# Kernel optimization log

Measured on AMD Instinct MI355X. Metric: run time of the kernel, lower is better.

The kernel has to match this reference:

```python
import jax, jax.numpy as jnp
import numpy as np

HEAD_DIM = 64
FEAT_H, FEAT_W = 64, 64
ROPE_THETA = 10000.0


def axial_rope_cache(dim, height, width, theta):
    # Matches compute_axial_rope_cache: interleaved cos/sin of shape [H*W, dim]
    theta_dim = (dim // 2) // 2
    freqs = 1.0 / theta ** (jnp.arange(theta_dim, dtype=jnp.float32) * 2.0 / theta_dim)
    t_x = jnp.tile(jnp.arange(width, dtype=jnp.float32)[None, :], (height, 1)).reshape(-1)
    t_y = jnp.tile(jnp.arange(height, dtype=jnp.float32)[:, None], (1, width)).reshape(-1)
    theta_all = jnp.concatenate([jnp.outer(t_x, freqs), jnp.outer(t_y, freqs)], axis=-1)
    cos = jnp.repeat(jnp.cos(theta_all), 2, axis=-1)  # [H*W, dim]
    sin = jnp.repeat(jnp.sin(theta_all), 2, axis=-1)
    return cos, sin


def apply_rope(x, cos, sin):
    # x: [B, H, N, D]; cos/sin: [N, D]
    x1 = x[..., 0::2]
    x2 = x[..., 1::2]
    rot = jnp.stack([-x2, x1], axis=-1).reshape(x.shape)
    return x * cos[None, None] + rot * sin[None, None]


def setup_inputs() -> dict:
    key = jax.random.key(0)
    ks = jax.random.split(key, 11)
    B, Nq, Nk, E, KVD, ID = 1, 4096, 8192, 256, 64, 256
    s_e = 1.0 / np.sqrt(E)
    s_kv = 1.0 / np.sqrt(KVD)
    s_i = 1.0 / np.sqrt(ID)
    return {
        "query": jax.random.normal(ks[0], (B, Nq, E), jnp.float32),
        "key": jax.random.normal(ks[1], (B, Nk, KVD), jnp.float32),
        "value": jax.random.normal(ks[2], (B, Nk, KVD), jnp.float32),
        "Wq": jax.random.normal(ks[3], (E, ID), jnp.float32) * s_e,
        "bq": jnp.zeros((ID,), jnp.float32),
        "Wk": jax.random.normal(ks[4], (KVD, ID), jnp.float32) * s_kv,
        "bk": jnp.zeros((ID,), jnp.float32),
        "Wv": jax.random.normal(ks[5], (KVD, ID), jnp.float32) * s_kv,
        "bv": jnp.zeros((ID,), jnp.float32),
        "Wo": jax.random.normal(ks[6], (ID, E), jnp.float32) * s_i,
        "bo": jnp.zeros((E,), jnp.float32),
        "num_k_exclude_rope": 0,
    }


def reference(query, key, value, Wq, bq, Wk, bk, Wv, bv, Wo, bo, num_k_exclude_rope):
    B, Nq, _ = query.shape
    Nk = key.shape[1]
    H, D = 4, HEAD_DIM

    def split_heads(x):
        b, n, c = x.shape
        return x.reshape(b, n, H, c // H).transpose(0, 2, 1, 3)

    q = split_heads(query @ Wq + bq)  # [B,H,Nq,D]
    k = split_heads(key @ Wk + bk)    # [B,H,Nk,D]
    v = split_heads(value @ Wv + bv)

    cos, sin = axial_rope_cache(D, FEAT_H, FEAT_W, ROPE_THETA)  # [4096, D]
    q = apply_rope(q, cos, sin)

    num_k_rope = Nk - num_k_exclude_rope
    k_spatial = k[:, :, :num_k_rope, :]
    k_other = k[:, :, num_k_rope:, :]
    repeats = num_k_rope // cos.shape[0]  # rope_k_repeat=True
    cos_k = jnp.tile(cos, (repeats, 1))
    sin_k = jnp.tile(sin, (repeats, 1))
    k_spatial = apply_rope(k_spatial, cos_k, sin_k)
    k = jnp.concatenate([k_spatial, k_other], axis=2)

    q = q / jnp.sqrt(jnp.asarray(D, q.dtype))
    scores = jnp.einsum("bhqd,bhkd->bhqk", q, k)
    attn = jax.nn.softmax(scores, axis=-1)
    out = jnp.einsum("bhqk,bhkd->bhqd", attn, v)
    out = out.transpose(0, 2, 1, 3).reshape(B, Nq, H * D)
    return out @ Wo + bo
```

## Files before the change

kernel.cpp:

```cpp
#include <hip/hip_runtime.h>
#include <hip/hip_bf16.h>

#define H 4
#define NQ 4096
#define NK 8192
#define D 64
#define BK 64
#define NSPLIT 8
#define KSPAN (NK / NSPLIT)
#define PST 72

#define QSCALE 0.1803368801111204f

typedef short v8s __attribute__((ext_vector_type(8)));
typedef float v4f __attribute__((ext_vector_type(4)));

static __device__ __forceinline__ unsigned short f2bf(float f) {
    unsigned int u = __float_as_uint(f);
    u = (u + 0x7FFFu + ((u >> 16) & 1u)) >> 16;
    return (unsigned short)u;
}
static __device__ __forceinline__ float bf2f(unsigned short h) {
    return __uint_as_float(((unsigned int)h) << 16);
}
static __device__ __forceinline__ unsigned int pkbf(float a, float b) {
    union { __hip_bfloat162 h; unsigned int u; } cv;
    cv.h = __float22bfloat162_rn(make_float2(a, b));
    return cv.u;
}
static __device__ __forceinline__ void split8(const float* a, v8s& hi, v8s& lo) {
#pragma unroll
    for (int j = 0; j < 8; ++j) {
        unsigned short h = f2bf(a[j]);
        hi[j] = (short)h;
        lo[j] = (short)f2bf(a[j] - bf2f(h));
    }
}
static __device__ __forceinline__ void dma16(const unsigned short* g, unsigned short* l) {
    __builtin_amdgcn_global_load_lds(
        (const __attribute__((address_space(1))) unsigned int*)(const void*)g,
        (__attribute__((address_space(3))) unsigned int*)(void*)l, 16, 0, 0);
}

__global__ __launch_bounds__(256) void wprep_kernel(
    const float* __restrict__ Wq, const float* __restrict__ Wk,
    const float* __restrict__ Wv, const float* __restrict__ Wo,
    unsigned short* __restrict__ Wqt, unsigned short* __restrict__ Wkt,
    unsigned short* __restrict__ Wvt, unsigned short* __restrict__ Wot)
{
    int i = blockIdx.x * 256 + threadIdx.x;
    const float* src; unsigned short* dst; int idx, sh;
    if (i < 65536)       { src = Wq; dst = Wqt; idx = i;          sh = 8; }
    else if (i < 81920)  { src = Wk; dst = Wkt; idx = i - 65536;  sh = 6; }
    else if (i < 98304)  { src = Wv; dst = Wvt; idx = i - 81920;  sh = 6; }
    else                 { src = Wo; dst = Wot; idx = i - 98304;  sh = 8; }
    const int K = 1 << sh;
    const int c = idx >> sh, e = idx & (K - 1);
    const float v = src[e * 256 + c];
    const unsigned short h = f2bf(v);
    dst[idx] = h;
    dst[idx + (K << 8)] = f2bf(v - bf2f(h));
}

__global__ __launch_bounds__(256) void qkv_kernel(
    const float* __restrict__ query, const float* __restrict__ key,
    const float* __restrict__ value,
    const unsigned short* __restrict__ Wqt, const unsigned short* __restrict__ Wkt,
    const unsigned short* __restrict__ Wvt,
    const float* __restrict__ bq, const float* __restrict__ bk,
    const float* __restrict__ bv,
    unsigned short* __restrict__ Qb, unsigned short* __restrict__ Kb,
    unsigned short* __restrict__ Vt, const int* __restrict__ nexp)
{
    const int b = blockIdx.x;
    const int t = threadIdx.x, w = t >> 6, lane = t & 63;
    const int quad = lane >> 4, l16 = lane & 15;
    const int colbase = w * 64;

    if (b < 128) {
        const int n0 = b * 32;
        v4f acc[2][4];
#pragma unroll
        for (int st = 0; st < 2; ++st)
#pragma unroll
            for (int ct = 0; ct < 4; ++ct) {
                const float bb = bq[colbase + ct * 16 + l16];
                acc[st][ct] = v4f{bb, bb, bb, bb};
            }
#pragma unroll
        for (int k0 = 0; k0 < 256; k0 += 32) {
            v8s ah[2], al[2];
#pragma unroll
            for (int st = 0; st < 2; ++st) {
                float av[8];
                const float* ar = query + (size_t)(n0 + st * 16 + l16) * 256 + k0 + quad * 8;
                *(float4*)av = *(const float4*)ar;
                *(float4*)(av + 4) = *(const float4*)(ar + 4);
                split8(av, ah[st], al[st]);
            }
#pragma unroll
            for (int ct = 0; ct < 4; ++ct) {
                const unsigned short* wp = Wqt + (size_t)(colbase + ct * 16 + l16) * 256 + k0 + quad * 8;
                const v8s wh = *(const v8s*)wp;
                const v8s wl = *(const v8s*)(wp + 65536);
#pragma unroll
                for (int st = 0; st < 2; ++st) {
                    acc[st][ct] = __builtin_amdgcn_mfma_f32_16x16x32_bf16(al[st], wh, acc[st][ct], 0, 0, 0);
                    acc[st][ct] = __builtin_amdgcn_mfma_f32_16x16x32_bf16(ah[st], wl, acc[st][ct], 0, 0, 0);
                    acc[st][ct] = __builtin_amdgcn_mfma_f32_16x16x32_bf16(ah[st], wh, acc[st][ct], 0, 0, 0);
                }
            }
        }
#pragma unroll
        for (int ct = 0; ct < 4; ++ct) {
            const int d = ct * 16 + l16;
            const int j = d >> 1;
            const float freq = exp2f(-(float)(j & 15) * 1.66096404744368f);
            const bool isx = (j < 16), odd = (d & 1);
#pragma unroll
            for (int st = 0; st < 2; ++st)
#pragma unroll
                for (int r = 0; r < 4; ++r) {
                    const int p = n0 + st * 16 + quad * 4 + r;
                    const float tpos = isx ? (float)(p & 63) : (float)(p >> 6);
                    float sn, cs;
                    __sincosf(tpos * freq, &sn, &cs);
                    const float x = acc[st][ct][r];
                    const float xp = __shfl_xor(x, 1, 64);
                    const float y = odd ? fmaf(x, cs, xp * sn) : fmaf(x, cs, -xp * sn);
                    Qb[((size_t)(w * NQ + p) << 6) + d] = f2bf(y * QSCALE);
                }
        }
    } else {
        const bool isK = (b < 384);
        const int n0 = (isK ? (b - 128) : (b - 384)) * 32;
        const float* X = isK ? key : value;
        const unsigned short* Wt = isK ? Wkt : Wvt;
        const float* bias = isK ? bk : bv;
        v8s wf[4][2][2];
#pragma unroll
        for (int ct = 0; ct < 4; ++ct)
#pragma unroll
            for (int k = 0; k < 2; ++k) {
                const unsigned short* wp = Wt + (size_t)(colbase + ct * 16 + l16) * 64 + k * 32 + quad * 8;
                wf[ct][k][0] = *(const v8s*)wp;
                wf[ct][k][1] = *(const v8s*)(wp + 16384);
            }
        v4f acc[2][4];
#pragma unroll
        for (int st = 0; st < 2; ++st)
#pragma unroll
            for (int ct = 0; ct < 4; ++ct) {
                const float bb = bias[colbase + ct * 16 + l16];
                acc[st][ct] = v4f{bb, bb, bb, bb};
            }
#pragma unroll
        for (int st = 0; st < 2; ++st)
#pragma unroll
            for (int k = 0; k < 2; ++k) {
                float av[8];
                const float* ar = X + (size_t)(n0 + st * 16 + l16) * 64 + k * 32 + quad * 8;
                *(float4*)av = *(const float4*)ar;
                *(float4*)(av + 4) = *(const float4*)(ar + 4);
                v8s ah, al;
                split8(av, ah, al);
#pragma unroll
                for (int ct = 0; ct < 4; ++ct) {
                    acc[st][ct] = __builtin_amdgcn_mfma_f32_16x16x32_bf16(al, wf[ct][k][0], acc[st][ct], 0, 0, 0);
                    acc[st][ct] = __builtin_amdgcn_mfma_f32_16x16x32_bf16(ah, wf[ct][k][1], acc[st][ct], 0, 0, 0);
                    acc[st][ct] = __builtin_amdgcn_mfma_f32_16x16x32_bf16(ah, wf[ct][k][0], acc[st][ct], 0, 0, 0);
                }
            }
        if (isK) {
            const int nro = NK - *nexp;
#pragma unroll
            for (int ct = 0; ct < 4; ++ct) {
                const int d = ct * 16 + l16;
                const int j = d >> 1;
                const float freq = exp2f(-(float)(j & 15) * 1.66096404744368f);
                const bool isx = (j < 16), odd = (d & 1);
#pragma unroll
                for (int st = 0; st < 2; ++st)
#pragma unroll
                    for (int r = 0; r < 4; ++r) {
                        const int p = n0 + st * 16 + quad * 4 + r;
                        const int pc = p & 4095;
                        const float tpos = isx ? (float)(pc & 63) : (float)(pc >> 6);
                        float sn, cs;
                        __sincosf(tpos * freq, &sn, &cs);
                        const float x = acc[st][ct][r];
                        const float xp = __shfl_xor(x, 1, 64);
                        float y = odd ? fmaf(x, cs, xp * sn) : fmaf(x, cs, -xp * sn);
                        y = (p < nro) ? y : x;
                        Kb[((size_t)(w * NK + p) << 6) + d] = f2bf(y);
                    }
            }
        } else {
#pragma unroll
            for (int ct = 0; ct < 4; ++ct) {
                const int col = colbase + ct * 16 + l16;
#pragma unroll
                for (int st = 0; st < 2; ++st) {
                    uint2 u = make_uint2(pkbf(acc[st][ct][0], acc[st][ct][1]),
                                         pkbf(acc[st][ct][2], acc[st][ct][3]));
                    *(uint2*)(Vt + (size_t)col * NK + n0 + st * 16 + quad * 4) = u;
                }
            }
        }
    }
}

__global__ __launch_bounds__(256) void attn_kernel(
    const unsigned short* __restrict__ Qb, const unsigned short* __restrict__ Kb,
    const unsigned short* __restrict__ Vt, unsigned short* __restrict__ Opart,
    float* __restrict__ Lbuf)
{
    __shared__ alignas(16) unsigned short Kl[64 * 64];
    __shared__ alignas(16) unsigned short Vl[64 * 64];
    __shared__ alignas(16) unsigned short Pl[4 * 32 * PST];

    const int blk = blockIdx.x;
    const int s = blk & 7, h = (blk >> 3) & 3, qt = blk >> 5;
    const int t = threadIdx.x;
    const int w = t >> 6, lane = t & 63;
    const int quad = lane >> 4, l16 = lane & 15;

    const int q0 = qt * 128 + w * 32;
    v8s qf[2][2];
#pragma unroll
    for (int g = 0; g < 2; ++g) {
        const unsigned short* qr = Qb + ((size_t)(h * NQ + q0 + g * 16 + l16) << 6) + quad * 8;
        qf[g][0] = *(const v8s*)qr;
        qf[g][1] = *(const v8s*)(qr + 32);
    }

    v4f O[4][2];
#pragma unroll
    for (int dt = 0; dt < 4; ++dt)
#pragma unroll
        for (int g = 0; g < 2; ++g) O[dt][g] = v4f{0.f, 0.f, 0.f, 0.f};
    float psum[2] = {0.f, 0.f};

    const unsigned short* Kbase = Kb + (((size_t)h * NK + s * KSPAN) << 6);
    const unsigned short* Vbase = Vt + (size_t)(h * 64) * NK + s * KSPAN;

    const int srow = lane >> 3;
    const int schunk = (lane & 7) ^ srow;
    const int c0off = ((quad ^ (l16 & 7)) * 8);
    const int c1off = c0off ^ 32;
    unsigned short* Pw = &Pl[w * 32 * PST];

    for (int k0 = 0; k0 < KSPAN; k0 += BK) {
        __syncthreads();
#pragma unroll
        for (int half = 0; half < 2; ++half) {
            const int r0 = w * 16 + half * 8;
            dma16(Kbase + ((size_t)(k0 + r0 + srow) << 6) + schunk * 8, &Kl[r0 * 64]);
            dma16(Vbase + (size_t)(r0 + srow) * NK + k0 + schunk * 8, &Vl[r0 * 64]);
        }
        __syncthreads();

#pragma unroll
        for (int tt = 0; tt < 4; ++tt) {
            const unsigned short* kr = &Kl[(tt * 16 + l16) * 64];
            const v8s kf0 = *(const v8s*)(kr + c0off);
            const v8s kf1 = *(const v8s*)(kr + c1off);
#pragma unroll
            for (int g = 0; g < 2; ++g) {
                v4f a = v4f{0.f, 0.f, 0.f, 0.f};
                a = __builtin_amdgcn_mfma_f32_16x16x32_bf16(kf0, qf[g][0], a, 0, 0, 0);
                a = __builtin_amdgcn_mfma_f32_16x16x32_bf16(kf1, qf[g][1], a, 0, 0, 0);
                const float e0 = __builtin_amdgcn_exp2f(a[0]);
                const float e1 = __builtin_amdgcn_exp2f(a[1]);
                const float e2 = __builtin_amdgcn_exp2f(a[2]);
                const float e3 = __builtin_amdgcn_exp2f(a[3]);
                psum[g] += (e0 + e1) + (e2 + e3);
                *(uint2*)(&Pw[(g * 16 + l16) * PST + tt * 16 + quad * 4]) =
                    make_uint2(pkbf(e0, e1), pkbf(e2, e3));
            }
        }
        __asm__ volatile("s_waitcnt lgkmcnt(0)" ::: "memory");

        v8s pf[2][2];
#pragma unroll
        for (int g = 0; g < 2; ++g) {
            const unsigned short* pr = &Pw[(g * 16 + l16) * PST + quad * 8];
            pf[g][0] = *(const v8s*)pr;
            pf[g][1] = *(const v8s*)(pr + 32);
        }
#pragma unroll
        for (int dt = 0; dt < 4; ++dt) {
            const unsigned short* vr = &Vl[(dt * 16 + l16) * 64];
            const v8s vf0 = *(const v8s*)(vr + c0off);
            const v8s vf1 = *(const v8s*)(vr + c1off);
#pragma unroll
            for (int g = 0; g < 2; ++g) {
                v4f a = O[dt][g];
                a = __builtin_amdgcn_mfma_f32_16x16x32_bf16(vf0, pf[g][0], a, 0, 0, 0);
                a = __builtin_amdgcn_mfma_f32_16x16x32_bf16(vf1, pf[g][1], a, 0, 0, 0);
                O[dt][g] = a;
            }
        }
    }

#pragma unroll
    for (int g = 0; g < 2; ++g) {
        float p = psum[g];
        p += __shfl_xor(p, 16, 64);
        p += __shfl_xor(p, 32, 64);
        psum[g] = p;
    }
    unsigned short* Ob = Opart + (size_t)blk * 8192;
#pragma unroll
    for (int g = 0; g < 2; ++g) {
        const int row = w * 32 + g * 16 + l16;
#pragma unroll
        for (int dt = 0; dt < 4; ++dt) {
            uint2 u = make_uint2(pkbf(O[dt][g][0], O[dt][g][1]),
                                 pkbf(O[dt][g][2], O[dt][g][3]));
            *(uint2*)(Ob + row * 64 + dt * 16 + quad * 4) = u;
        }
        if (quad == 0) Lbuf[blk * 128 + row] = psum[g];
    }
}

__global__ __launch_bounds__(256) void oproj_kernel(
    const unsigned short* __restrict__ Opart, const float* __restrict__ Lbuf,
    const unsigned short* __restrict__ Wt, const float* __restrict__ bo,
    float* __restrict__ out)
{
    const int t = threadIdx.x, w = t >> 6, lane = t & 63;
    const int quad = lane >> 4, l16 = lane & 15;
    const int n0 = blockIdx.x * 16, colbase = w * 64;
    const int qt = n0 >> 7, rbase = n0 & 127;

    v4f facc[4];
#pragma unroll
    for (int ct = 0; ct < 4; ++ct) facc[ct] = v4f{0.f, 0.f, 0.f, 0.f};

#pragma unroll 1
    for (int hh = 0; hh < 4; ++hh) {
        v8s wfr[4][2][2];
#pragma unroll
        for (int ct = 0; ct < 4; ++ct)
#pragma unroll
            for (int ch = 0; ch < 2; ++ch) {
                const unsigned short* wp = Wt + (size_t)(colbase + ct * 16 + l16) * 256 + hh * 64 + ch * 32 + quad * 8;
                wfr[ct][ch][0] = *(const v8s*)wp;
                wfr[ct][ch][1] = *(const v8s*)(wp + 65536);
            }
        v4f hacc[4];
#pragma unroll
        for (int ct = 0; ct < 4; ++ct) hacc[ct] = v4f{0.f, 0.f, 0.f, 0.f};
        float4 lsum = make_float4(0.f, 0.f, 0.f, 0.f);
#pragma unroll
        for (int sp = 0; sp < NSPLIT; ++sp) {
            const int slab = (qt * 4 + hh) * 8 + sp;
            const unsigned short* arow = Opart + (size_t)slab * 8192 + (rbase + l16) * 64;
#pragma unroll
            for (int ch = 0; ch < 2; ++ch) {
                const v8s A = *(const v8s*)(arow + ch * 32 + quad * 8);
#pragma unroll
                for (int ct = 0; ct < 4; ++ct) {
                    hacc[ct] = __builtin_amdgcn_mfma_f32_16x16x32_bf16(A, wfr[ct][ch][0], hacc[ct], 0, 0, 0);
                    hacc[ct] = __builtin_amdgcn_mfma_f32_16x16x32_bf16(A, wfr[ct][ch][1], hacc[ct], 0, 0, 0);
                }
            }
            const float4 lv = *(const float4*)(Lbuf + slab * 128 + rbase + quad * 4);
            lsum.x += lv.x; lsum.y += lv.y; lsum.z += lv.z; lsum.w += lv.w;
        }
        const float li[4] = {1.f / lsum.x, 1.f / lsum.y, 1.f / lsum.z, 1.f / lsum.w};
#pragma unroll
        for (int ct = 0; ct < 4; ++ct)
#pragma unroll
            for (int r = 0; r < 4; ++r)
                facc[ct][r] = fmaf(hacc[ct][r], li[r], facc[ct][r]);
    }
#pragma unroll
    for (int ct = 0; ct < 4; ++ct) {
        const float bb = bo[colbase + ct * 16 + l16];
#pragma unroll
        for (int r = 0; r < 4; ++r)
            out[(size_t)(n0 + quad * 4 + r) * 256 + colbase + ct * 16 + l16] = facc[ct][r] + bb;
    }
}

extern "C" void kernel_launch(void* const* d_in, const int* in_sizes, int n_in,
                              void* d_out, int out_size, void* d_ws, size_t ws_size,
                              hipStream_t stream) {
    const float* query = (const float*)d_in[0];
    const float* key   = (const float*)d_in[1];
    const float* value = (const float*)d_in[2];
    const float* Wq    = (const float*)d_in[3];
    const float* bq    = (const float*)d_in[4];
    const float* Wk    = (const float*)d_in[5];
    const float* bk    = (const float*)d_in[6];
    const float* Wv    = (const float*)d_in[7];
    const float* bv    = (const float*)d_in[8];
    const float* Wo    = (const float*)d_in[9];
    const float* bo    = (const float*)d_in[10];
    const int*   nex   = (const int*)d_in[11];

    char* ws = (char*)d_ws;
    unsigned short* Qb  = (unsigned short*)(ws);
    unsigned short* Kb  = (unsigned short*)(ws + (size_t)2  * 1024 * 1024);
    unsigned short* Vt  = (unsigned short*)(ws + (size_t)6  * 1024 * 1024);
    unsigned short* Opart = (unsigned short*)(ws + (size_t)10 * 1024 * 1024);
    float* Lbuf         = (float*)(ws + (size_t)26 * 1024 * 1024);
    char* wbase         = ws + (size_t)26 * 1024 * 1024 + 512 * 1024;
    unsigned short* Wqt = (unsigned short*)(wbase);
    unsigned short* Wkt = (unsigned short*)(wbase + 256 * 1024);
    unsigned short* Wvt = (unsigned short*)(wbase + 320 * 1024);
    unsigned short* Wot = (unsigned short*)(wbase + 384 * 1024);
    float* out          = (float*)d_out;

    wprep_kernel<<<640, 256, 0, stream>>>(Wq, Wk, Wv, Wo, Wqt, Wkt, Wvt, Wot);
    qkv_kernel<<<640, 256, 0, stream>>>(query, key, value, Wqt, Wkt, Wvt,
                                        bq, bk, bv, Qb, Kb, Vt, nex);
    attn_kernel<<<1024, 256, 0, stream>>>(Qb, Kb, Vt, Opart, Lbuf);
    oproj_kernel<<<256, 256, 0, stream>>>(Opart, Lbuf, Wot, bo, out);
}
```

Measured before the change: 180.2 us.

## Drop weight-prep kernel, gather fp32 weights inline, retile attention and output projection

Removes the separate weight transpose/split kernel. The QKV and output-projection kernels now gather the fp32 weights with strided loads and split them into bf16 hi/lo on the fly. The QKV grid halves rows per block (doubling the block count), and attention uses 128-thread blocks with 64 query rows per wave. The output projection uses 512 threads, splits the heads across two wave halves and reduces them through shared memory. This saves a kernel launch and its memory round-trip, but adds uncoalesced strided weight reads and redundant conversion work in every block.

```diff
diff --git a/kernel.cpp b/kernel.cpp
--- a/kernel.cpp
+++ b/kernel.cpp
@@ -1,13 +1,11 @@
 #include <hip/hip_runtime.h>
 #include <hip/hip_bf16.h>
 
-#define H 4
 #define NQ 4096
 #define NK 8192
-#define D 64
-#define BK 64
 #define NSPLIT 8
 #define KSPAN (NK / NSPLIT)
+#define BK 64
 #define PST 72
 
 #define QSCALE 0.1803368801111204f
@@ -36,37 +34,24 @@
         lo[j] = (short)f2bf(a[j] - bf2f(h));
     }
 }
+static __device__ __forceinline__ void wgather(const float* __restrict__ W,
+                                               int k0, int col, v8s& wh, v8s& wl) {
+    float wv[8];
+#pragma unroll
+    for (int j = 0; j < 8; ++j) wv[j] = W[(size_t)(k0 + j) * 256 + col];
+    split8(wv, wh, wl);
+}
 static __device__ __forceinline__ void dma16(const unsigned short* g, unsigned short* l) {
     __builtin_amdgcn_global_load_lds(
         (const __attribute__((address_space(1))) unsigned int*)(const void*)g,
         (__attribute__((address_space(3))) unsigned int*)(void*)l, 16, 0, 0);
 }
 
-__global__ __launch_bounds__(256) void wprep_kernel(
-    const float* __restrict__ Wq, const float* __restrict__ Wk,
-    const float* __restrict__ Wv, const float* __restrict__ Wo,
-    unsigned short* __restrict__ Wqt, unsigned short* __restrict__ Wkt,
-    unsigned short* __restrict__ Wvt, unsigned short* __restrict__ Wot)
-{
-    int i = blockIdx.x * 256 + threadIdx.x;
-    const float* src; unsigned short* dst; int idx, sh;
-    if (i < 65536)       { src = Wq; dst = Wqt; idx = i;          sh = 8; }
-    else if (i < 81920)  { src = Wk; dst = Wkt; idx = i - 65536;  sh = 6; }
-    else if (i < 98304)  { src = Wv; dst = Wvt; idx = i - 81920;  sh = 6; }
-    else                 { src = Wo; dst = Wot; idx = i - 98304;  sh = 8; }
-    const int K = 1 << sh;
-    const int c = idx >> sh, e = idx & (K - 1);
-    const float v = src[e * 256 + c];
-    const unsigned short h = f2bf(v);
-    dst[idx] = h;
-    dst[idx + (K << 8)] = f2bf(v - bf2f(h));
-}
-
 __global__ __launch_bounds__(256) void qkv_kernel(
     const float* __restrict__ query, const float* __restrict__ key,
     const float* __restrict__ value,
-    const unsigned short* __restrict__ Wqt, const unsigned short* __restrict__ Wkt,
-    const unsigned short* __restrict__ Wvt,
+    const float* __restrict__ Wq, const float* __restrict__ Wk,
+    const float* __restrict__ Wv,
     const float* __restrict__ bq, const float* __restrict__ bk,
     const float* __restrict__ bv,
     unsigned short* __restrict__ Qb, unsigned short* __restrict__ Kb,
@@ -77,38 +62,29 @@
     const int quad = lane >> 4, l16 = lane & 15;
     const int colbase = w * 64;
 
-    if (b < 128) {
-        const int n0 = b * 32;
-        v4f acc[2][4];
-#pragma unroll
-        for (int st = 0; st < 2; ++st)
+    if (b < 256) {
+        const int n0 = b * 16;
+        v4f acc[4];
+#pragma unroll
+        for (int ct = 0; ct < 4; ++ct) {
+            const float bb = bq[colbase + ct * 16 + l16];
+            acc[ct] = v4f{bb, bb, bb, bb};
+        }
+        const float* arow = query + (size_t)(n0 + l16) * 256 + quad * 8;
+#pragma unroll
+        for (int k0 = 0; k0 < 256; k0 += 32) {
+            float av[8];
+            *(float4*)av = *(const float4*)(arow + k0);
+            *(float4*)(av + 4) = *(const float4*)(arow + k0 + 4);
+            v8s ah, al;
+            split8(av, ah, al);
 #pragma unroll
             for (int ct = 0; ct < 4; ++ct) {
-                const float bb = bq[colbase + ct * 16 + l16];
-                acc[st][ct] = v4f{bb, bb, bb, bb};
-            }
-#pragma unroll
-        for (int k0 = 0; k0 < 256; k0 += 32) {
-            v8s ah[2], al[2];
-#pragma unroll
-            for (int st = 0; st < 2; ++st) {
-                float av[8];
-                const float* ar = query + (size_t)(n0 + st * 16 + l16) * 256 + k0 + quad * 8;
-                *(float4*)av = *(const float4*)ar;
-                *(float4*)(av + 4) = *(const float4*)(ar + 4);
-                split8(av, ah[st], al[st]);
-            }
-#pragma unroll
-            for (int ct = 0; ct < 4; ++ct) {
-                const unsigned short* wp = Wqt + (size_t)(colbase + ct * 16 + l16) * 256 + k0 + quad * 8;
-                const v8s wh = *(const v8s*)wp;
-                const v8s wl = *(const v8s*)(wp + 65536);
-#pragma unroll
-                for (int st = 0; st < 2; ++st) {
-                    acc[st][ct] = __builtin_amdgcn_mfma_f32_16x16x32_bf16(al[st], wh, acc[st][ct], 0, 0, 0);
-                    acc[st][ct] = __builtin_amdgcn_mfma_f32_16x16x32_bf16(ah[st], wl, acc[st][ct], 0, 0, 0);
-                    acc[st][ct] = __builtin_amdgcn_mfma_f32_16x16x32_bf16(ah[st], wh, acc[st][ct], 0, 0, 0);
-                }
+                v8s wh, wl;
+                wgather(Wq, k0 + quad * 8, colbase + ct * 16 + l16, wh, wl);
+                acc[ct] = __builtin_amdgcn_mfma_f32_16x16x32_bf16(al, wh, acc[ct], 0, 0, 0);
+                acc[ct] = __builtin_amdgcn_mfma_f32_16x16x32_bf16(ah, wl, acc[ct], 0, 0, 0);
+                acc[ct] = __builtin_amdgcn_mfma_f32_16x16x32_bf16(ah, wh, acc[ct], 0, 0, 0);
             }
         }
 #pragma unroll
@@ -118,59 +94,46 @@
             const float freq = exp2f(-(float)(j & 15) * 1.66096404744368f);
             const bool isx = (j < 16), odd = (d & 1);
 #pragma unroll
-            for (int st = 0; st < 2; ++st)
-#pragma unroll
-                for (int r = 0; r < 4; ++r) {
-                    const int p = n0 + st * 16 + quad * 4 + r;
-                    const float tpos = isx ? (float)(p & 63) : (float)(p >> 6);
-                    float sn, cs;
-                    __sincosf(tpos * freq, &sn, &cs);
-                    const float x = acc[st][ct][r];
-                    const float xp = __shfl_xor(x, 1, 64);
-                    const float y = odd ? fmaf(x, cs, xp * sn) : fmaf(x, cs, -xp * sn);
-                    Qb[((size_t)(w * NQ + p) << 6) + d] = f2bf(y * QSCALE);
-                }
+            for (int r = 0; r < 4; ++r) {
+                const int p = n0 + quad * 4 + r;
+                const float tpos = isx ? (float)(p & 63) : (float)(p >> 6);
+                float sn, cs;
+                __sincosf(tpos * freq, &sn, &cs);
+                const float x = acc[ct][r];
+                const float xp = __shfl_xor(x, 1, 64);
+                const float y = odd ? fmaf(x, cs, xp * sn) : fmaf(x, cs, -xp * sn);
+                Qb[((size_t)(w * NQ + p) << 6) + d] = f2bf(y * QSCALE);
+            }
         }
     } else {
-        const bool isK = (b < 384);
-        const int n0 = (isK ? (b - 128) : (b - 384)) * 32;
+        const bool isK = (b < 768);
+        const int n0 = (isK ? (b - 256) : (b - 768)) * 16;
         const float* X = isK ? key : value;
-        const unsigned short* Wt = isK ? Wkt : Wvt;
+        const float* W = isK ? Wk : Wv;
         const float* bias = isK ? bk : bv;
-        v8s wf[4][2][2];
-#pragma unroll
-        for (int ct = 0; ct < 4; ++ct)
-#pragma unroll
-            for (int k = 0; k < 2; ++k) {
-                const unsigned short* wp = Wt + (size_t)(colbase + ct * 16 + l16) * 64 + k * 32 + quad * 8;
-                wf[ct][k][0] = *(const v8s*)wp;
-                wf[ct][k][1] = *(const v8s*)(wp + 16384);
-            }
-        v4f acc[2][4];
-#pragma unroll
-        for (int st = 0; st < 2; ++st)
+        v4f acc[4];
+#pragma unroll
+        for (int ct = 0; ct < 4; ++ct) {
+            const float bb = bias[colbase + ct * 16 + l16];
+            acc[ct] = v4f{bb, bb, bb, bb};
+        }
+        const float* arow = X + (size_t)(n0 + l16) * 64 + quad * 8;
+#pragma unroll
+        for (int k0 = 0; k0 < 64; k0 += 32) {
+            float av[8];
+            *(float4*)av = *(const float4*)(arow + k0);
+            *(float4*)(av + 4) = *(const float4*)(arow + k0 + 4);
+            v8s ah, al;
+            split8(av, ah, al);
 #pragma unroll
             for (int ct = 0; ct < 4; ++ct) {
-                const float bb = bias[colbase + ct * 16 + l16];
-                acc[st][ct] = v4f{bb, bb, bb, bb};
-            }
-#pragma unroll
-        for (int st = 0; st < 2; ++st)
-#pragma unroll
-            for (int k = 0; k < 2; ++k) {
-                float av[8];
-                const float* ar = X + (size_t)(n0 + st * 16 + l16) * 64 + k * 32 + quad * 8;
-                *(float4*)av = *(const float4*)ar;
-                *(float4*)(av + 4) = *(const float4*)(ar + 4);
-                v8s ah, al;
-                split8(av, ah, al);
-#pragma unroll
-                for (int ct = 0; ct < 4; ++ct) {
-                    acc[st][ct] = __builtin_amdgcn_mfma_f32_16x16x32_bf16(al, wf[ct][k][0], acc[st][ct], 0, 0, 0);
-                    acc[st][ct] = __builtin_amdgcn_mfma_f32_16x16x32_bf16(ah, wf[ct][k][1], acc[st][ct], 0, 0, 0);
-                    acc[st][ct] = __builtin_amdgcn_mfma_f32_16x16x32_bf16(ah, wf[ct][k][0], acc[st][ct], 0, 0, 0);
-                }
-            }
+                v8s wh, wl;
+                wgather(W, k0 + quad * 8, colbase + ct * 16 + l16, wh, wl);
+                acc[ct] = __builtin_amdgcn_mfma_f32_16x16x32_bf16(al, wh, acc[ct], 0, 0, 0);
+                acc[ct] = __builtin_amdgcn_mfma_f32_16x16x32_bf16(ah, wl, acc[ct], 0, 0, 0);
+                acc[ct] = __builtin_amdgcn_mfma_f32_16x16x32_bf16(ah, wh, acc[ct], 0, 0, 0);
+            }
+        }
         if (isK) {
             const int nro = NK - *nexp;
 #pragma unroll
@@ -180,44 +143,39 @@
                 const float freq = exp2f(-(float)(j & 15) * 1.66096404744368f);
                 const bool isx = (j < 16), odd = (d & 1);
 #pragma unroll
-                for (int st = 0; st < 2; ++st)
-#pragma unroll
-                    for (int r = 0; r < 4; ++r) {
-                        const int p = n0 + st * 16 + quad * 4 + r;
-                        const int pc = p & 4095;
-                        const float tpos = isx ? (float)(pc & 63) : (float)(pc >> 6);
-                        float sn, cs;
-                        __sincosf(tpos * freq, &sn, &cs);
-                        const float x = acc[st][ct][r];
-                        const float xp = __shfl_xor(x, 1, 64);
-                        float y = odd ? fmaf(x, cs, xp * sn) : fmaf(x, cs, -xp * sn);
-                        y = (p < nro) ? y : x;
-                        Kb[((size_t)(w * NK + p) << 6) + d] = f2bf(y);
-                    }
+                for (int r = 0; r < 4; ++r) {
+                    const int p = n0 + quad * 4 + r;
+                    const int pc = p & 4095;
+                    const float tpos = isx ? (float)(pc & 63) : (float)(pc >> 6);
+                    float sn, cs;
+                    __sincosf(tpos * freq, &sn, &cs);
+                    const float x = acc[ct][r];
+                    const float xp = __shfl_xor(x, 1, 64);
+                    float y = odd ? fmaf(x, cs, xp * sn) : fmaf(x, cs, -xp * sn);
+                    y = (p < nro) ? y : x;
+                    Kb[((size_t)(w * NK + p) << 6) + d] = f2bf(y);
+                }
             }
         } else {
 #pragma unroll
             for (int ct = 0; ct < 4; ++ct) {
                 const int col = colbase + ct * 16 + l16;
-#pragma unroll
-                for (int st = 0; st < 2; ++st) {
-                    uint2 u = make_uint2(pkbf(acc[st][ct][0], acc[st][ct][1]),
-                                         pkbf(acc[st][ct][2], acc[st][ct][3]));
-                    *(uint2*)(Vt + (size_t)col * NK + n0 + st * 16 + quad * 4) = u;
-                }
-            }
-        }
-    }
-}
-
-__global__ __launch_bounds__(256) void attn_kernel(
+                uint2 u = make_uint2(pkbf(acc[ct][0], acc[ct][1]),
+                                     pkbf(acc[ct][2], acc[ct][3]));
+                *(uint2*)(Vt + (size_t)col * NK + n0 + quad * 4) = u;
+            }
+        }
+    }
+}
+
+__global__ __launch_bounds__(128) void attn_kernel(
     const unsigned short* __restrict__ Qb, const unsigned short* __restrict__ Kb,
     const unsigned short* __restrict__ Vt, unsigned short* __restrict__ Opart,
     float* __restrict__ Lbuf)
 {
     __shared__ alignas(16) unsigned short Kl[64 * 64];
     __shared__ alignas(16) unsigned short Vl[64 * 64];
-    __shared__ alignas(16) unsigned short Pl[4 * 32 * PST];
+    __shared__ alignas(16) unsigned short Pl[2 * 64 * PST];
 
     const int blk = blockIdx.x;
     const int s = blk & 7, h = (blk >> 3) & 3, qt = blk >> 5;
@@ -225,21 +183,21 @@
     const int w = t >> 6, lane = t & 63;
     const int quad = lane >> 4, l16 = lane & 15;
 
-    const int q0 = qt * 128 + w * 32;
-    v8s qf[2][2];
-#pragma unroll
-    for (int g = 0; g < 2; ++g) {
+    const int q0 = qt * 128 + w * 64;
+    v8s qf[4][2];
+#pragma unroll
+    for (int g = 0; g < 4; ++g) {
         const unsigned short* qr = Qb + ((size_t)(h * NQ + q0 + g * 16 + l16) << 6) + quad * 8;
         qf[g][0] = *(const v8s*)qr;
         qf[g][1] = *(const v8s*)(qr + 32);
     }
 
-    v4f O[4][2];
+    v4f O[4][4];
 #pragma unroll
     for (int dt = 0; dt < 4; ++dt)
 #pragma unroll
-        for (int g = 0; g < 2; ++g) O[dt][g] = v4f{0.f, 0.f, 0.f, 0.f};
-    float psum[2] = {0.f, 0.f};
+        for (int g = 0; g < 4; ++g) O[dt][g] = v4f{0.f, 0.f, 0.f, 0.f};
+    float psum[4] = {0.f, 0.f, 0.f, 0.f};
 
     const unsigned short* Kbase = Kb + (((size_t)h * NK + s * KSPAN) << 6);
     const unsigned short* Vbase = Vt + (size_t)(h * 64) * NK + s * KSPAN;
@@ -248,13 +206,13 @@
     const int schunk = (lane & 7) ^ srow;
     const int c0off = ((quad ^ (l16 & 7)) * 8);
     const int c1off = c0off ^ 32;
-    unsigned short* Pw = &Pl[w * 32 * PST];
+    unsigned short* Pw = &Pl[w * 64 * PST];
 
     for (int k0 = 0; k0 < KSPAN; k0 += BK) {
         __syncthreads();
 #pragma unroll
-        for (int half = 0; half < 2; ++half) {
-            const int r0 = w * 16 + half * 8;
+        for (int half = 0; half < 4; ++half) {
+            const int r0 = w * 32 + half * 8;
             dma16(Kbase + ((size_t)(k0 + r0 + srow) << 6) + schunk * 8, &Kl[r0 * 64]);
             dma16(Vbase + (size_t)(r0 + srow) * NK + k0 + schunk * 8, &Vl[r0 * 64]);
         }
@@ -266,7 +224,7 @@
             const v8s kf0 = *(const v8s*)(kr + c0off);
             const v8s kf1 = *(const v8s*)(kr + c1off);
 #pragma unroll
-            for (int g = 0; g < 2; ++g) {
+            for (int g = 0; g < 4; ++g) {
                 v4f a = v4f{0.f, 0.f, 0.f, 0.f};
                 a = __builtin_amdgcn_mfma_f32_16x16x32_bf16(kf0, qf[g][0], a, 0, 0, 0);
                 a = __builtin_amdgcn_mfma_f32_16x16x32_bf16(kf1, qf[g][1], a, 0, 0, 0);
@@ -281,9 +239,9 @@
         }
         __asm__ volatile("s_waitcnt lgkmcnt(0)" ::: "memory");
 
-        v8s pf[2][2];
-#pragma unroll
-        for (int g = 0; g < 2; ++g) {
+        v8s pf[4][2];
+#pragma unroll
+        for (int g = 0; g < 4; ++g) {
             const unsigned short* pr = &Pw[(g * 16 + l16) * PST + quad * 8];
             pf[g][0] = *(const v8s*)pr;
             pf[g][1] = *(const v8s*)(pr + 32);
@@ -294,7 +252,7 @@
             const v8s vf0 = *(const v8s*)(vr + c0off);
             const v8s vf1 = *(const v8s*)(vr + c1off);
 #pragma unroll
-            for (int g = 0; g < 2; ++g) {
+            for (int g = 0; g < 4; ++g) {
                 v4f a = O[dt][g];
                 a = __builtin_amdgcn_mfma_f32_16x16x32_bf16(vf0, pf[g][0], a, 0, 0, 0);
                 a = __builtin_amdgcn_mfma_f32_16x16x32_bf16(vf1, pf[g][1], a, 0, 0, 0);
@@ -304,7 +262,7 @@
     }
 
 #pragma unroll
-    for (int g = 0; g < 2; ++g) {
+    for (int g = 0; g < 4; ++g) {
         float p = psum[g];
         p += __shfl_xor(p, 16, 64);
         p += __shfl_xor(p, 32, 64);
@@ -312,8 +270,8 @@
     }
     unsigned short* Ob = Opart + (size_t)blk * 8192;
 #pragma unroll
-    for (int g = 0; g < 2; ++g) {
-        const int row = w * 32 + g * 16 + l16;
+    for (int g = 0; g < 4; ++g) {
+        const int row = w * 64 + g * 16 + l16;
 #pragma unroll
         for (int dt = 0; dt < 4; ++dt) {
             uint2 u = make_uint2(pkbf(O[dt][g][0], O[dt][g][1]),
@@ -324,46 +282,47 @@
     }
 }
 
-__global__ __launch_bounds__(256) void oproj_kernel(
+__global__ __launch_bounds__(512) void oproj_kernel(
     const unsigned short* __restrict__ Opart, const float* __restrict__ Lbuf,
-    const unsigned short* __restrict__ Wt, const float* __restrict__ bo,
+    const float* __restrict__ Wo, const float* __restrict__ bo,
     float* __restrict__ out)
 {
+    __shared__ float Ex[2][16][256];
     const int t = threadIdx.x, w = t >> 6, lane = t & 63;
     const int quad = lane >> 4, l16 = lane & 15;
-    const int n0 = blockIdx.x * 16, colbase = w * 64;
+    const int n0 = blockIdx.x * 16;
+    const int colbase = (w & 3) * 64;
     const int qt = n0 >> 7, rbase = n0 & 127;
 
     v4f facc[4];
 #pragma unroll
     for (int ct = 0; ct < 4; ++ct) facc[ct] = v4f{0.f, 0.f, 0.f, 0.f};
 
-#pragma unroll 1
-    for (int hh = 0; hh < 4; ++hh) {
-        v8s wfr[4][2][2];
+#pragma unroll
+    for (int hhi = 0; hhi < 2; ++hhi) {
+        const int hh = (w >> 2) * 2 + hhi;
+        v8s wh[4][2], wl[4][2];
 #pragma unroll
         for (int ct = 0; ct < 4; ++ct)
 #pragma unroll
-            for (int ch = 0; ch < 2; ++ch) {
-                const unsigned short* wp = Wt + (size_t)(colbase + ct * 16 + l16) * 256 + hh * 64 + ch * 32 + quad * 8;
-                wfr[ct][ch][0] = *(const v8s*)wp;
-                wfr[ct][ch][1] = *(const v8s*)(wp + 65536);
-            }
+            for (int ch = 0; ch < 2; ++ch)
+                wgather(Wo, hh * 64 + ch * 32 + quad * 8, colbase + ct * 16 + l16,
+                        wh[ct][ch], wl[ct][ch]);
         v4f hacc[4];
 #pragma unroll
         for (int ct = 0; ct < 4; ++ct) hacc[ct] = v4f{0.f, 0.f, 0.f, 0.f};
         float4 lsum = make_float4(0.f, 0.f, 0.f, 0.f);
 #pragma unroll
         for (int sp = 0; sp < NSPLIT; ++sp) {
-            const int slab = (qt * 4 + hh) * 8 + sp;
+            const int slab = qt * 32 + hh * 8 + sp;
             const unsigned short* arow = Opart + (size_t)slab * 8192 + (rbase + l16) * 64;
 #pragma unroll
             for (int ch = 0; ch < 2; ++ch) {
                 const v8s A = *(const v8s*)(arow + ch * 32 + quad * 8);
 #pragma unroll
                 for (int ct = 0; ct < 4; ++ct) {
-                    hacc[ct] = __builtin_amdgcn_mfma_f32_16x16x32_bf16(A, wfr[ct][ch][0], hacc[ct], 0, 0, 0);
-                    hacc[ct] = __builtin_amdgcn_mfma_f32_16x16x32_bf16(A, wfr[ct][ch][1], hacc[ct], 0, 0, 0);
+                    hacc[ct] = __builtin_amdgcn_mfma_f32_16x16x32_bf16(A, wh[ct][ch], hacc[ct], 0, 0, 0);
+                    hacc[ct] = __builtin_amdgcn_mfma_f32_16x16x32_bf16(A, wl[ct][ch], hacc[ct], 0, 0, 0);
                 }
             }
             const float4 lv = *(const float4*)(Lbuf + slab * 128 + rbase + quad * 4);
@@ -376,12 +335,26 @@
             for (int r = 0; r < 4; ++r)
                 facc[ct][r] = fmaf(hacc[ct][r], li[r], facc[ct][r]);
     }
-#pragma unroll
-    for (int ct = 0; ct < 4; ++ct) {
-        const float bb = bo[colbase + ct * 16 + l16];
+    const int half = w >> 2;
+#pragma unroll
+    for (int ct = 0; ct < 4; ++ct)
 #pragma unroll
         for (int r = 0; r < 4; ++r)
-            out[(size_t)(n0 + quad * 4 + r) * 256 + colbase + ct * 16 + l16] = facc[ct][r] + bb;
+            Ex[half][quad * 4 + r][colbase + ct * 16 + l16] = facc[ct][r];
+    __syncthreads();
+    const int row = t >> 5, c0 = (t & 31) * 8;
+#pragma unroll
+    for (int g = 0; g < 2; ++g) {
+        const int c = c0 + g * 4;
+        const float4 x0 = *(const float4*)(&Ex[0][row][c]);
+        const float4 x1 = *(const float4*)(&Ex[1][row][c]);
+        const float4 bb = *(const float4*)(bo + c);
+        float4 o;
+        o.x = x0.x + x1.x + bb.x;
+        o.y = x0.y + x1.y + bb.y;
+        o.z = x0.z + x1.z + bb.z;
+        o.w = x0.w + x1.w + bb.w;
+        *(float4*)(out + (size_t)(n0 + row) * 256 + c) = o;
     }
 }
 
@@ -402,21 +375,15 @@
     const int*   nex   = (const int*)d_in[11];
 
     char* ws = (char*)d_ws;
-    unsigned short* Qb  = (unsigned short*)(ws);
-    unsigned short* Kb  = (unsigned short*)(ws + (size_t)2  * 1024 * 1024);
-    unsigned short* Vt  = (unsigned short*)(ws + (size_t)6  * 1024 * 1024);
+    unsigned short* Qb    = (unsigned short*)(ws);
+    unsigned short* Kb    = (unsigned short*)(ws + (size_t)2  * 1024 * 1024);
+    unsigned short* Vt    = (unsigned short*)(ws + (size_t)6  * 1024 * 1024);
     unsigned short* Opart = (unsigned short*)(ws + (size_t)10 * 1024 * 1024);
-    float* Lbuf         = (float*)(ws + (size_t)26 * 1024 * 1024);
-    char* wbase         = ws + (size_t)26 * 1024 * 1024 + 512 * 1024;
-    unsigned short* Wqt = (unsigned short*)(wbase);
-    unsigned short* Wkt = (unsigned short*)(wbase + 256 * 1024);
-    unsigned short* Wvt = (unsigned short*)(wbase + 320 * 1024);
-    unsigned short* Wot = (unsigned short*)(wbase + 384 * 1024);
-    float* out          = (float*)d_out;
-
-    wprep_kernel<<<640, 256, 0, stream>>>(Wq, Wk, Wv, Wo, Wqt, Wkt, Wvt, Wot);
-    qkv_kernel<<<640, 256, 0, stream>>>(query, key, value, Wqt, Wkt, Wvt,
-                                        bq, bk, bv, Qb, Kb, Vt, nex);
-    attn_kernel<<<1024, 256, 0, stream>>>(Qb, Kb, Vt, Opart, Lbuf);
-    oproj_kernel<<<256, 256, 0, stream>>>(Opart, Lbuf, Wot, bo, out);
-}
+    float* Lbuf           = (float*)(ws + (size_t)26 * 1024 * 1024);
+    float* out            = (float*)d_out;
+
+    qkv_kernel<<<1280, 256, 0, stream>>>(query, key, value, Wq, Wk, Wv,
+                                         bq, bk, bv, Qb, Kb, Vt, nex);
+    attn_kernel<<<1024, 128, 0, stream>>>(Qb, Kb, Vt, Opart, Lbuf);
+    oproj_kernel<<<256, 512, 0, stream>>>(Opart, Lbuf, Wo, bo, out);
+}
```

Result: slower. 189.8 us (+5.3%).
